# Performance work log

Measured on AMD Instinct MI355X. Metric: run time of the kernel, lower is better.

Reference implementation:

```python
import jax, jax.numpy as jnp
from jax import lax
import numpy as np

LATENT = 16
HIDDEN = 16  # latent_dim > 8 -> 16
NUM_ATTRACTORS = 64
GRAVITY = 0.01
INPUT_DIM = 300
B, S = 32, 2048
N_ITERS = 20


def setup_inputs() -> dict:
    key = jax.random.key(0)
    ks = jax.random.split(key, 12)
    sc = lambda fan_in: 1.0 / np.sqrt(fan_in)
    return {
        "inputs": jax.random.normal(ks[0], (B, S, INPUT_DIM), dtype=jnp.float32),
        "enc_w1": jax.random.normal(ks[1], (INPUT_DIM, HIDDEN), dtype=jnp.float32) * sc(INPUT_DIM),
        "enc_b1": jnp.zeros((HIDDEN,), dtype=jnp.float32),
        "enc_w2": jax.random.normal(ks[2], (HIDDEN, LATENT), dtype=jnp.float32) * sc(HIDDEN),
        "enc_b2": jnp.zeros((LATENT,), dtype=jnp.float32),
        "attractors": jax.random.normal(ks[3], (NUM_ATTRACTORS, LATENT), dtype=jnp.float32) * 0.1,
        "dec_w1": jax.random.normal(ks[4], (LATENT, HIDDEN), dtype=jnp.float32) * sc(LATENT),
        "dec_b1": jnp.zeros((HIDDEN,), dtype=jnp.float32),
        "dec_w2": jax.random.normal(ks[5], (HIDDEN, INPUT_DIM), dtype=jnp.float32) * sc(HIDDEN),
        "dec_b2": jnp.zeros((INPUT_DIM,), dtype=jnp.float32),
        "mass_w": jax.random.normal(ks[6], (LATENT, 1), dtype=jnp.float32) * sc(LATENT),
        "mass_b": jnp.zeros((1,), dtype=jnp.float32),
    }


def reference(inputs, enc_w1, enc_b1, enc_w2, enc_b2, attractors,
              dec_w1, dec_b1, dec_w2, dec_b2, mass_w, mass_b):
    b, s, _ = inputs.shape
    # encoder: Linear(300,16) -> ReLU -> Linear(16,latent)
    h = jax.nn.relu(jnp.einsum('bsi,ih->bsh', inputs, enc_w1) + enc_b1)
    emb = jnp.einsum('bsh,hd->bsd', h, enc_w2) + enc_b2  # [B,S,D]

    def step(pos, _):
        # pos: [B,S,D]; attractors: [A,D]
        diff = attractors[None, None, :, :] - pos[:, :, None, :]          # [B,S,A,D]
        dist = jnp.sqrt(jnp.sum(diff * diff, axis=-1, keepdims=True)) + 1e-6
        forces = jnp.sum(GRAVITY * diff / (dist * dist), axis=2)          # [B,S,D]
        new_pos = pos + 0.1 * forces
        change = jnp.sqrt(jnp.sum((new_pos - pos) ** 2))
        return new_pos, change

    # torch code breaks if change < 1e-6; with random data this never fires,
    # so the fixed 20-iteration scan is equivalent.
    positions, changes = lax.scan(step, emb, None, length=N_ITERS)

    attractor_field = positions.mean(axis=1)                              # [B,D]
    rec = jax.nn.relu(attractor_field @ dec_w1 + dec_b1) @ dec_w2 + dec_b2  # [B,300]
    reconstructions = jnp.broadcast_to(rec[:, None, :], (b, s, INPUT_DIM))
    masses = jax.nn.sigmoid(attractor_field @ mass_w + mass_b)            # [B,1]
    final_change = changes[-1]
    return attractor_field, reconstructions, masses, final_change
```

## Files before the change

kernel.cpp:

```cpp
#include <hip/hip_runtime.h>
#include <cmath>

#define BB 32
#define SS 2048
#define IND 300
#define HID 16
#define LAT 16
#define NA 64
#define NITER 20
#define GRAV 0.01f

#define OFF_FIELD 0
#define OFF_REC   512
#define OFF_MASS  (512 + BB*SS*IND)
#define OFF_CHG   (OFF_MASS + BB)

#define WS_FIELD 0
#define WS_CHG   512

typedef __attribute__((ext_vector_type(8))) __bf16 bf16x8;
typedef __attribute__((ext_vector_type(4))) __bf16 bf16x4;
typedef __attribute__((ext_vector_type(4))) float f32x4;

#define HST 40
#define WTS 88

__global__ __launch_bounds__(256, 4)
void k_fused(const float* __restrict__ x,  const float* __restrict__ w1,
             const float* __restrict__ b1, const float* __restrict__ w2,
             const float* __restrict__ b2, const float* __restrict__ att,
             float* __restrict__ ws)
{
    __shared__ __align__(16) __bf16 Wl[4][16 * WTS];
    __shared__ __align__(16) __bf16 hl[4][16 * HST];
    __shared__ float red[4][LAT];
    __shared__ float redc[4];

    const int tid  = threadIdx.x;
    const int wave = tid >> 6, lane = tid & 63;
    const int quad = lane >> 4, col = lane & 15;
    const int tok  = blockIdx.x * 64 + wave * 16 + col;

    f32x4 p;
    {
        const float* xr = x + (size_t)tok * IND;
        const float b1c = b1[col];
        f32x4 hacc = {b1c, b1c, b1c, b1c};

        #pragma unroll
        for (int s = 0; s < 9; ++s) {
            const float* xp = xr + s * 32 + quad * 8;
            f32x4 lo = *(const f32x4*)(xp);
            f32x4 hi = *(const f32x4*)(xp + 4);
            bf16x8 af, wf;
            #pragma unroll
            for (int e = 0; e < 4; ++e) { af[e] = (__bf16)lo[e]; af[4 + e] = (__bf16)hi[e]; }
            #pragma unroll
            for (int j = 0; j < 8; ++j)
                wf[j] = (__bf16)w1[(s * 32 + quad * 8 + j) * HID + col];
            hacc = __builtin_amdgcn_mfma_f32_16x16x32_bf16(af, wf, hacc, 0, 0, 0);
        }
        {
            bf16x8 af, wf;
            #pragma unroll
            for (int e = 0; e < 8; ++e) af[e] = (__bf16)0.f;
            if (quad == 0) {
                f32x4 lo = *(const f32x4*)(xr + 288);
                f32x4 hi = *(const f32x4*)(xr + 292);
                #pragma unroll
                for (int e = 0; e < 4; ++e) { af[e] = (__bf16)lo[e]; af[4 + e] = (__bf16)hi[e]; }
            } else if (quad == 1) {
                f32x4 lo = *(const f32x4*)(xr + 296);
                #pragma unroll
                for (int e = 0; e < 4; ++e) af[e] = (__bf16)lo[e];
            }
            #pragma unroll
            for (int j = 0; j < 8; ++j) {
                const int k = 288 + quad * 8 + j;
                wf[j] = (k < IND) ? (__bf16)w1[k * HID + col] : (__bf16)0.f;
            }
            hacc = __builtin_amdgcn_mfma_f32_16x16x32_bf16(af, wf, hacc, 0, 0, 0);
        }

        __bf16* myh = hl[wave];
        #pragma unroll
        for (int r = 0; r < 4; ++r)
            myh[(quad * 4 + r) * HST + col] = (__bf16)fmaxf(hacc[r], 0.f);

        bf16x8 w2tf;
        #pragma unroll
        for (int j = 0; j < 8; ++j) {
            const int k = quad * 8 + j;
            w2tf[j] = (k < HID) ? (__bf16)w2[k * LAT + col] : (__bf16)0.f;
        }
        bf16x8 bh;
        #pragma unroll
        for (int e = 0; e < 8; ++e) bh[e] = (__bf16)0.f;
        if (quad < 2)
            bh = *(const bf16x8*)(myh + col * HST + quad * 8);
        f32x4 pacc = *(const f32x4*)(b2 + quad * 4);
        p = __builtin_amdgcn_mfma_f32_16x16x32_bf16(w2tf, bh, pacc, 0, 0, 0);
    }

    const f32x4 zf = {0.f, 0.f, 0.f, 0.f};
    bf16x8 ones8;
    #pragma unroll
    for (int e = 0; e < 8; ++e) ones8[e] = (__bf16)1.0f;

    bf16x8 aS[4];
    #pragma unroll
    for (int i = 0; i < 4; ++i) {
        f32x4 av = *(const f32x4*)(att + (16 * i + col) * LAT + quad * 4);
        #pragma unroll
        for (int m = 0; m < 4; ++m) {
            aS[i][2 * m]     = (__bf16)(-2.0f * av[m]);
            aS[i][2 * m + 1] = (__bf16)1.0f;
        }
    }
    f32x4 sanv[4];
    {
        float nrm[4];
        #pragma unroll
        for (int i = 0; i < 4; ++i) {
            const float* ar = att + (16 * i + col) * LAT;
            float s = 0.f;
            #pragma unroll
            for (int k = 0; k < LAT; ++k) s = fmaf(ar[k], ar[k], s);
            nrm[i] = s;
        }
        #pragma unroll
        for (int i = 0; i < 4; ++i)
            #pragma unroll
            for (int r = 0; r < 4; ++r)
                sanv[i][r] = __shfl(nrm[i], 16 * quad + quad * 4 + r);
    }
    bf16x8 aF[2];
    #pragma unroll
    for (int h = 0; h < 2; ++h)
        #pragma unroll
        for (int j = 0; j < 8; ++j)
            aF[h][j] = (__bf16)att[(32 * h + quad * 8 + j) * LAT + col];

    __bf16* myW = Wl[wave];
    float cd = 0.f;

    #pragma unroll 1
    for (int it = 0; it < NITER; ++it) {
        bf16x8 bp;
        #pragma unroll
        for (int m = 0; m < 4; ++m) {
            float v = p[m];
            bp[2 * m]     = (__bf16)v;
            bp[2 * m + 1] = (__bf16)(v * v);
        }
        f32x4 sf[4];
        #pragma unroll
        for (int i = 0; i < 4; ++i)
            sf[i] = __builtin_amdgcn_mfma_f32_16x16x32_bf16(aS[i], bp, zf, 0, 0, 0);

        #pragma unroll
        for (int i = 0; i < 4; ++i) {
            bf16x4 wp;
            #pragma unroll
            for (int r = 0; r < 4; ++r)
                wp[r] = (__bf16)__builtin_amdgcn_rcpf(sf[i][r] + sanv[i][r]);
            *(bf16x4*)(myW + col * WTS + 16 * i + quad * 4) = wp;
        }
        bf16x8 bw0 = *(const bf16x8*)(myW + col * WTS + quad * 8);
        bf16x8 bw1 = *(const bf16x8*)(myW + col * WTS + 32 + quad * 8);

        f32x4 F  = __builtin_amdgcn_mfma_f32_16x16x32_bf16(aF[0], bw0, zf, 0, 0, 0);
        F  = __builtin_amdgcn_mfma_f32_16x16x32_bf16(aF[1], bw1, F,  0, 0, 0);
        f32x4 F2 = __builtin_amdgcn_mfma_f32_16x16x32_bf16(ones8, bw0, zf, 0, 0, 0);
        F2 = __builtin_amdgcn_mfma_f32_16x16x32_bf16(ones8, bw1, F2, 0, 0, 0);

        const bool last = (it == NITER - 1);
        #pragma unroll
        for (int r = 0; r < 4; ++r) {
            float np = fmaf(p[r], fmaf(F2[r], -0.1f * GRAV, 1.0f),
                            (0.1f * GRAV) * F[r]);
            if (last) { float d = np - p[r]; cd = fmaf(d, d, cd); }
            p[r] = np;
        }
    }

    f32x4 fs = p;
    #pragma unroll
    for (int m = 1; m <= 8; m <<= 1)
        #pragma unroll
        for (int r = 0; r < 4; ++r) fs[r] += __shfl_xor(fs[r], m);
    if (col == 0) {
        #pragma unroll
        for (int r = 0; r < 4; ++r) red[wave][quad * 4 + r] = fs[r];
    }
    float c2 = cd;
    c2 += __shfl_xor(c2, 1);  c2 += __shfl_xor(c2, 2);  c2 += __shfl_xor(c2, 4);
    c2 += __shfl_xor(c2, 8);  c2 += __shfl_xor(c2, 16); c2 += __shfl_xor(c2, 32);
    if (lane == 0) redc[wave] = c2;
    __syncthreads();

    const int b = blockIdx.x >> 5;
    if (tid < LAT) {
        float v = red[0][tid] + red[1][tid] + red[2][tid] + red[3][tid];
        atomicAdd(ws + WS_FIELD + b * LAT + tid, v);
    }
    if (tid == 32)
        atomicAdd(ws + WS_CHG, redc[0] + redc[1] + redc[2] + redc[3]);
}

#define CHUNK 8192
#define CPB   (SS * IND / CHUNK)
__global__ __launch_bounds__(256)
void k_bcast(const float* __restrict__ dw1, const float* __restrict__ db1,
             const float* __restrict__ dw2, const float* __restrict__ db2,
             const float* __restrict__ mw,  const float* __restrict__ mb,
             const float* __restrict__ ws, float* __restrict__ out)
{
    __shared__ float sf[LAT];
    __shared__ float sh[HID];
    __shared__ __align__(16) float srow[IND];
    const int blk = blockIdx.x;
    const int b = blk / CPB, c = blk % CPB;
    const int t = threadIdx.x;

    if (t < LAT) {
        float f = ws[WS_FIELD + b * LAT + t] * (1.f / SS);
        sf[t] = f;
        if (c == 0) out[OFF_FIELD + b * LAT + t] = f;
    }
    __syncthreads();
    if (t < HID) {
        float a = db1[t];
        #pragma unroll
        for (int d = 0; d < LAT; ++d) a = fmaf(sf[d], dw1[d * HID + t], a);
        sh[t] = fmaxf(a, 0.f);
    }
    if (c == 0 && t == 32) {
        float a = mb[0];
        #pragma unroll
        for (int d = 0; d < LAT; ++d) a = fmaf(sf[d], mw[d], a);
        out[OFF_MASS + b] = 1.f / (1.f + expf(-a));
    }
    if (blk == 0 && t == 33) out[OFF_CHG] = sqrtf(ws[WS_CHG]);
    __syncthreads();
    if (t < IND) {
        float a = db2[t];
        #pragma unroll
        for (int j = 0; j < HID; ++j) a = fmaf(sh[j], dw2[j * IND + t], a);
        srow[t] = a;
    }
    if (t < IND - 256) {
        const int tc = t + 256;
        float a2 = db2[tc];
        #pragma unroll
        for (int j = 0; j < HID; ++j) a2 = fmaf(sh[j], dw2[j * IND + tc], a2);
        srow[tc] = a2;
    }
    __syncthreads();
    f32x4* o = (f32x4*)(out + OFF_REC + (size_t)b * (SS * IND) + (size_t)c * CHUNK);
    #pragma unroll
    for (int i = 0; i < CHUNK / 4 / 256; ++i) {
        const int o4 = i * 256 + t;
        const int r  = (c * CHUNK + o4 * 4) % IND;
        f32x4 v = *(const f32x4*)(srow + r);
        __builtin_nontemporal_store(v, o + o4);
    }
}

extern "C" void kernel_launch(void* const* d_in, const int* in_sizes, int n_in,
                              void* d_out, int out_size, void* d_ws, size_t ws_size,
                              hipStream_t stream)
{
    const float* x   = (const float*)d_in[0];
    const float* ew1 = (const float*)d_in[1];
    const float* eb1 = (const float*)d_in[2];
    const float* ew2 = (const float*)d_in[3];
    const float* eb2 = (const float*)d_in[4];
    const float* att = (const float*)d_in[5];
    const float* dw1 = (const float*)d_in[6];
    const float* db1 = (const float*)d_in[7];
    const float* dw2 = (const float*)d_in[8];
    const float* db2 = (const float*)d_in[9];
    const float* mw  = (const float*)d_in[10];
    const float* mb  = (const float*)d_in[11];
    float* out = (float*)d_out;
    float* ws  = (float*)d_ws;

    (void)hipMemsetAsync(ws, 0, (WS_CHG + 1) * sizeof(float), stream);
    k_fused<<<BB * SS / 64, 256, 0, stream>>>(x, ew1, eb1, ew2, eb2, att, ws);
    k_bcast<<<BB * CPB, 256, 0, stream>>>(dw1, db1, dw2, db2, mw, mb, ws, out);
}
```

Measured before the change: 190.3 us.

## Use ds_bpermute for weight transpose, preload x tile, spread change atomics

Replaces the per-iteration shared-memory round trip that transposes the reciprocal weights between MFMA layouts with packed bf16 pairs exchanged through ds_bpermute lane shuffles. It also issues all global loads of the input row before the encoder MFMA chain so the memory requests can overlap, and spreads the global change-accumulator atomic over 64 slots that the broadcast kernel sums. This removes LDS traffic and the single-address atomic contention, but adds register pressure from holding the 20 preloaded vectors and eight bpermutes per iteration.

```diff
diff --git a/kernel.cpp b/kernel.cpp
--- a/kernel.cpp
+++ b/kernel.cpp
@@ -20,10 +20,16 @@
 
 typedef __attribute__((ext_vector_type(8))) __bf16 bf16x8;
 typedef __attribute__((ext_vector_type(4))) __bf16 bf16x4;
+typedef __attribute__((ext_vector_type(2))) __bf16 bf16x2;
 typedef __attribute__((ext_vector_type(4))) float f32x4;
+typedef __attribute__((ext_vector_type(4))) unsigned uint4v;
 
 #define HST 40
-#define WTS 88
+
+__device__ __forceinline__ unsigned pk_bf16(float lo, float hi) {
+    bf16x2 t; t[0] = (__bf16)lo; t[1] = (__bf16)hi;
+    return __builtin_bit_cast(unsigned, t);
+}
 
 __global__ __launch_bounds__(256, 4)
 void k_fused(const float* __restrict__ x,  const float* __restrict__ w1,
@@ -31,7 +37,6 @@
              const float* __restrict__ b2, const float* __restrict__ att,
              float* __restrict__ ws)
 {
-    __shared__ __align__(16) __bf16 Wl[4][16 * WTS];
     __shared__ __align__(16) __bf16 hl[4][16 * HST];
     __shared__ float red[4][LAT];
     __shared__ float redc[4];
@@ -44,40 +49,45 @@
     f32x4 p;
     {
         const float* xr = x + (size_t)tok * IND;
+
+        f32x4 xv[10][2];
+        #pragma unroll
+        for (int s = 0; s < 9; ++s) {
+            const float* xp = xr + s * 32 + quad * 8;
+            xv[s][0] = *(const f32x4*)(xp);
+            xv[s][1] = *(const f32x4*)(xp + 4);
+        }
+        {
+            const f32x4 z = {0.f, 0.f, 0.f, 0.f};
+            xv[9][0] = z; xv[9][1] = z;
+            if (quad == 0) {
+                xv[9][0] = *(const f32x4*)(xr + 288);
+                xv[9][1] = *(const f32x4*)(xr + 292);
+            } else if (quad == 1) {
+                xv[9][0] = *(const f32x4*)(xr + 296);
+            }
+        }
+
         const float b1c = b1[col];
         f32x4 hacc = {b1c, b1c, b1c, b1c};
-
-        #pragma unroll
-        for (int s = 0; s < 9; ++s) {
-            const float* xp = xr + s * 32 + quad * 8;
-            f32x4 lo = *(const f32x4*)(xp);
-            f32x4 hi = *(const f32x4*)(xp + 4);
+        #pragma unroll
+        for (int s = 0; s < 10; ++s) {
             bf16x8 af, wf;
             #pragma unroll
-            for (int e = 0; e < 4; ++e) { af[e] = (__bf16)lo[e]; af[4 + e] = (__bf16)hi[e]; }
-            #pragma unroll
-            for (int j = 0; j < 8; ++j)
-                wf[j] = (__bf16)w1[(s * 32 + quad * 8 + j) * HID + col];
-            hacc = __builtin_amdgcn_mfma_f32_16x16x32_bf16(af, wf, hacc, 0, 0, 0);
-        }
-        {
-            bf16x8 af, wf;
-            #pragma unroll
-            for (int e = 0; e < 8; ++e) af[e] = (__bf16)0.f;
-            if (quad == 0) {
-                f32x4 lo = *(const f32x4*)(xr + 288);
-                f32x4 hi = *(const f32x4*)(xr + 292);
+            for (int e = 0; e < 4; ++e) {
+                af[e]     = (__bf16)xv[s][0][e];
+                af[4 + e] = (__bf16)xv[s][1][e];
+            }
+            if (s < 9) {
                 #pragma unroll
-                for (int e = 0; e < 4; ++e) { af[e] = (__bf16)lo[e]; af[4 + e] = (__bf16)hi[e]; }
-            } else if (quad == 1) {
-                f32x4 lo = *(const f32x4*)(xr + 296);
+                for (int j = 0; j < 8; ++j)
+                    wf[j] = (__bf16)w1[(s * 32 + quad * 8 + j) * HID + col];
+            } else {
                 #pragma unroll
-                for (int e = 0; e < 4; ++e) af[e] = (__bf16)lo[e];
-            }
-            #pragma unroll
-            for (int j = 0; j < 8; ++j) {
-                const int k = 288 + quad * 8 + j;
-                wf[j] = (k < IND) ? (__bf16)w1[k * HID + col] : (__bf16)0.f;
+                for (int j = 0; j < 8; ++j)
+                    wf[j] = (quad * 8 + j < 12)
+                          ? (__bf16)w1[(288 + quad * 8 + j) * HID + col]
+                          : (__bf16)0.f;
             }
             hacc = __builtin_amdgcn_mfma_f32_16x16x32_bf16(af, wf, hacc, 0, 0, 0);
         }
@@ -141,9 +151,11 @@
         for (int j = 0; j < 8; ++j)
             aF[h][j] = (__bf16)att[(32 * h + quad * 8 + j) * LAT + col];
 
-    __bf16* myW = Wl[wave];
+    const int bpA0 = (((quad & 1) * 32) + col) * 4;
+    const int bpA1 = bpA0 + 64;
+    const bool qhi = (quad & 2) != 0;
+
     float cd = 0.f;
-
     #pragma unroll 1
     for (int it = 0; it < NITER; ++it) {
         bf16x8 bp;
@@ -158,16 +170,34 @@
         for (int i = 0; i < 4; ++i)
             sf[i] = __builtin_amdgcn_mfma_f32_16x16x32_bf16(aS[i], bp, zf, 0, 0, 0);
 
+        unsigned sd0[4], sd1[4];
         #pragma unroll
         for (int i = 0; i < 4; ++i) {
-            bf16x4 wp;
-            #pragma unroll
-            for (int r = 0; r < 4; ++r)
-                wp[r] = (__bf16)__builtin_amdgcn_rcpf(sf[i][r] + sanv[i][r]);
-            *(bf16x4*)(myW + col * WTS + 16 * i + quad * 4) = wp;
-        }
-        bf16x8 bw0 = *(const bf16x8*)(myW + col * WTS + quad * 8);
-        bf16x8 bw1 = *(const bf16x8*)(myW + col * WTS + 32 + quad * 8);
+            float w0 = __builtin_amdgcn_rcpf(sf[i][0] + sanv[i][0]);
+            float w1_ = __builtin_amdgcn_rcpf(sf[i][1] + sanv[i][1]);
+            float w2_ = __builtin_amdgcn_rcpf(sf[i][2] + sanv[i][2]);
+            float w3_ = __builtin_amdgcn_rcpf(sf[i][3] + sanv[i][3]);
+            sd0[i] = pk_bf16(w0, w1_);
+            sd1[i] = pk_bf16(w2_, w3_);
+        }
+        unsigned ra0 = qhi ? sd0[1] : sd0[0];
+        unsigned rb0 = qhi ? sd1[1] : sd1[0];
+        unsigned ra1 = qhi ? sd0[3] : sd0[2];
+        unsigned rb1 = qhi ? sd1[3] : sd1[2];
+
+        int b0 = __builtin_amdgcn_ds_bpermute(bpA0, (int)ra0);
+        int b1v = __builtin_amdgcn_ds_bpermute(bpA0, (int)rb0);
+        int b2v = __builtin_amdgcn_ds_bpermute(bpA1, (int)ra0);
+        int b3 = __builtin_amdgcn_ds_bpermute(bpA1, (int)rb0);
+        int b4 = __builtin_amdgcn_ds_bpermute(bpA0, (int)ra1);
+        int b5 = __builtin_amdgcn_ds_bpermute(bpA0, (int)rb1);
+        int b6 = __builtin_amdgcn_ds_bpermute(bpA1, (int)ra1);
+        int b7 = __builtin_amdgcn_ds_bpermute(bpA1, (int)rb1);
+
+        uint4v u0 = {(unsigned)b0, (unsigned)b1v, (unsigned)b2v, (unsigned)b3};
+        uint4v u1 = {(unsigned)b4, (unsigned)b5, (unsigned)b6, (unsigned)b7};
+        bf16x8 bw0 = __builtin_bit_cast(bf16x8, u0);
+        bf16x8 bw1 = __builtin_bit_cast(bf16x8, u1);
 
         f32x4 F  = __builtin_amdgcn_mfma_f32_16x16x32_bf16(aF[0], bw0, zf, 0, 0, 0);
         F  = __builtin_amdgcn_mfma_f32_16x16x32_bf16(aF[1], bw1, F,  0, 0, 0);
@@ -205,7 +235,8 @@
         atomicAdd(ws + WS_FIELD + b * LAT + tid, v);
     }
     if (tid == 32)
-        atomicAdd(ws + WS_CHG, redc[0] + redc[1] + redc[2] + redc[3]);
+        atomicAdd(ws + WS_CHG + (blockIdx.x & 63),
+                  redc[0] + redc[1] + redc[2] + redc[3]);
 }
 
 #define CHUNK 8192
@@ -218,6 +249,7 @@
 {
     __shared__ float sf[LAT];
     __shared__ float sh[HID];
+    __shared__ float schg[64];
     __shared__ __align__(16) float srow[IND];
     const int blk = blockIdx.x;
     const int b = blk / CPB, c = blk % CPB;
@@ -228,6 +260,7 @@
         sf[t] = f;
         if (c == 0) out[OFF_FIELD + b * LAT + t] = f;
     }
+    if (blk == 0 && t < 64) schg[t] = ws[WS_CHG + t];
     __syncthreads();
     if (t < HID) {
         float a = db1[t];
@@ -241,7 +274,12 @@
         for (int d = 0; d < LAT; ++d) a = fmaf(sf[d], mw[d], a);
         out[OFF_MASS + b] = 1.f / (1.f + expf(-a));
     }
-    if (blk == 0 && t == 33) out[OFF_CHG] = sqrtf(ws[WS_CHG]);
+    if (blk == 0 && t == 33) {
+        float s = 0.f;
+        #pragma unroll
+        for (int i = 0; i < 64; ++i) s += schg[i];
+        out[OFF_CHG] = sqrtf(s);
+    }
     __syncthreads();
     if (t < IND) {
         float a = db2[t];
@@ -286,7 +324,7 @@
     float* out = (float*)d_out;
     float* ws  = (float*)d_ws;
 
-    (void)hipMemsetAsync(ws, 0, (WS_CHG + 1) * sizeof(float), stream);
+    (void)hipMemsetAsync(ws, 0, (WS_CHG + 64) * sizeof(float), stream);
     k_fused<<<BB * SS / 64, 256, 0, stream>>>(x, ew1, eb1, ew2, eb2, att, ws);
     k_bcast<<<BB * CPB, 256, 0, stream>>>(dw1, db1, dw2, db2, mw, mb, ws, out);
 }
```

Result: no change. 192.9 us (+1.4%).
